# Kernel tuning notes

Measured on AMD Instinct MI355X. Metric: run time of the kernel, lower is better.

The kernel has to match this reference:

```python
import jax, jax.numpy as jnp
import numpy as np

HEADS = 16
DIM_HEAD = 64


def setup_inputs() -> dict:
    key = jax.random.key(0)
    k1, k2, k3 = jax.random.split(key, 3)
    b, n, dim = 4, 2048, 1024
    inner = HEADS * DIM_HEAD  # 1024
    x = jax.random.normal(k1, (b, n, dim), dtype=jnp.float32)
    # Dense weights, scaled like Glorot-ish init to keep softmax well-behaved
    w_qkv = jax.random.normal(k2, (dim, 3 * inner), dtype=jnp.float32) * (dim ** -0.5)
    w_out = jax.random.normal(k3, (inner, dim), dtype=jnp.float32) * (inner ** -0.5)
    b_out = jnp.zeros((dim,), dtype=jnp.float32)
    return {"x": x, "w_qkv": w_qkv, "w_out": w_out, "b_out": b_out}


def reference(x, w_qkv, w_out, b_out):
    b, n, dim = x.shape
    scale = DIM_HEAD ** -0.5
    qkv = x @ w_qkv  # [b, n, 3*h*d]
    q, k, v = jnp.split(qkv, 3, axis=-1)
    # 'b n (h d) -> b h n d'
    split_heads = lambda t: t.reshape(b, n, HEADS, DIM_HEAD).transpose(0, 2, 1, 3)
    q, k, v = split_heads(q), split_heads(k), split_heads(v)
    sim = jnp.einsum('bhid,bhjd->bhij', q, k) * scale  # [b, h, n, n]
    attn = jax.nn.softmax(sim, axis=-1)
    out = jnp.einsum('bhij,bhjd->bhid', attn, v)  # [b, h, n, d]
    out = out.transpose(0, 2, 1, 3).reshape(b, n, HEADS * DIM_HEAD)
    return out @ w_out + b_out  # dropout rate 0.0 -> identity
```

## Files before the change

kernel.cpp:

```cpp
#include <hip/hip_runtime.h>
#include <cstdint>

#define HEADS 16
#define DH 64
#define SEQ 2048
#define BATCH 4
#define DIM 1024
#define MTOT (BATCH*SEQ)
#define NQKV (3*DIM)

typedef short bf16x8 __attribute__((ext_vector_type(8)));
typedef float f32x4 __attribute__((ext_vector_type(4)));
typedef float f32x16 __attribute__((ext_vector_type(16)));

__device__ __forceinline__ unsigned short f2bf(float f) {
  union { float fv; unsigned int u; } c; c.fv = f;
  unsigned int u = c.u;
  u += 0x7FFFu + ((u >> 16) & 1u);
  return (unsigned short)(u >> 16);
}

__device__ __forceinline__ unsigned int cvtpk(float lo, float hi) {
  unsigned int r;
  asm("v_cvt_pk_bf16_f32 %0, %1, %2" : "=v"(r) : "v"(lo), "v"(hi));
  return r;
}

__device__ __forceinline__ f32x4 mfma16(bf16x8 a, bf16x8 b, f32x4 c) {
  return __builtin_amdgcn_mfma_f32_16x16x32_bf16(a, b, c, 0, 0, 0);
}
__device__ __forceinline__ f32x16 mfma32(bf16x8 a, bf16x8 b, f32x16 c) {
  return __builtin_amdgcn_mfma_f32_32x32x16_bf16(a, b, c, 0, 0, 0);
}

typedef const __attribute__((address_space(1))) unsigned int* gas_ptr;
typedef __attribute__((address_space(3))) unsigned int* las_ptr;
__device__ __forceinline__ void gl2lds16(const void* g, void* l) {
  __builtin_amdgcn_global_load_lds((gas_ptr)g, (las_ptr)l, 16, 0, 0);
}

#define QSCALE 0.18033688011112042f

__global__ __launch_bounds__(256) void cast_f32_bf16(
    const float* __restrict__ in, unsigned short* __restrict__ out, int n4) {
  int i = blockIdx.x * blockDim.x + threadIdx.x;
  if (i >= n4) return;
  float4 v = reinterpret_cast<const float4*>(in)[i];
  uint2 o;
  o.x = (unsigned int)f2bf(v.x) | ((unsigned int)f2bf(v.y) << 16);
  o.y = (unsigned int)f2bf(v.z) | ((unsigned int)f2bf(v.w) << 16);
  reinterpret_cast<uint2*>(out)[i] = o;
}

__global__ __launch_bounds__(256) void transpose_cast(
    const float* __restrict__ in, unsigned short* __restrict__ out, int R, int C) {
  __shared__ float tile[32][33];
  int c0 = blockIdx.x * 32, r0 = blockIdx.y * 32;
  int tx = threadIdx.x & 31, ty = threadIdx.x >> 5;
  for (int i = 0; i < 32; i += 8)
    tile[ty + i][tx] = in[(size_t)(r0 + ty + i) * C + c0 + tx];
  __syncthreads();
  for (int i = 0; i < 32; i += 8)
    out[(size_t)(c0 + ty + i) * R + r0 + tx] = f2bf(tile[tx][ty + i]);
}

__global__ __launch_bounds__(256) void transpose_v(
    const unsigned short* __restrict__ V, unsigned short* __restrict__ Vt) {
  __shared__ unsigned short tile[64][72];
  int n0 = blockIdx.x * 64;
  size_t base = (size_t)blockIdx.y * SEQ * DH;
  int t = threadIdx.x;
  int r = t >> 2, c = (t & 3) * 8;
  *(uint4*)&tile[r][c]      = *(const uint4*)&V[base + (size_t)(n0 + r) * DH + c];
  *(uint4*)&tile[r][c + 32] = *(const uint4*)&V[base + (size_t)(n0 + r) * DH + c + 32];
  __syncthreads();
#pragma unroll
  for (int p = 0; p < 2; p++) {
    alignas(16) unsigned short tmp[8];
#pragma unroll
    for (int i = 0; i < 8; i++) tmp[i] = tile[c + p * 32 + i][r];
    *(uint4*)&Vt[base + (size_t)r * SEQ + n0 + c + p * 32] = *(uint4*)tmp;
  }
}


#define STAGE(TT) { \
    char* _b = (char*)smem + ((TT) & 3) * 24576 + w * 1024; \
    gl2lds16(gA0 + (size_t)(TT) * 32, _b); \
    gl2lds16(gA1 + (size_t)(TT) * 32, _b + 8192); \
    gl2lds16(gB0 + (size_t)(TT) * 32, _b + 16384); }

#define WAITB(N) { \
    asm volatile("s_waitcnt vmcnt(" #N ")" ::: "memory"); \
    __builtin_amdgcn_s_barrier(); \
    __builtin_amdgcn_sched_barrier(0); }

#define GCOMPUTE(T) { \
    const unsigned short* sAt = smem + ((T) & 3) * 12288; \
    const unsigned short* sBt = sAt + 8192; \
    bf16x8 af[4], bv[4]; \
    _Pragma("unroll") \
    for (int mt = 0; mt < 4; mt++) \
      af[mt] = *reinterpret_cast<const bf16x8*>( \
          &sAt[(wr64 + mt * 16 + fr) * 32 + fchunk]); \
    _Pragma("unroll") \
    for (int nt = 0; nt < 4; nt++) \
      bv[nt] = *reinterpret_cast<const bf16x8*>( \
          &sBt[(wc64 + nt * 16 + fr) * 32 + fchunk]); \
    __builtin_amdgcn_s_setprio(1); \
    _Pragma("unroll") \
    for (int mt = 0; mt < 4; mt++) \
      _Pragma("unroll") \
      for (int nt = 0; nt < 4; nt++) \
        acc[mt][nt] = mfma16(af[mt], bv[nt], acc[mt][nt]); \
    __builtin_amdgcn_s_setprio(0); }

#define GEMM_SETUP(Abase, Bbase) \
  const int KD = 1024; \
  int t = threadIdx.x; \
  int lane = t & 63, w = t >> 6; \
  int wr64 = (w >> 1) * 64;            \
  int wc64 = (w & 1) * 64;             \
  int fr = lane & 15, fg = lane >> 4; \
  int fchunk = (fg ^ ((fr >> 1) & 3)) * 8;    \
  int lr = lane >> 2; \
  int cg = ((lane & 3) ^ ((lane >> 3) & 3)) * 8;   \
  const unsigned short* gA0 = (Abase) + (size_t)(m0 + w * 16 + lr) * KD + cg; \
  const unsigned short* gA1 = gA0 + (size_t)128 * KD; \
  const unsigned short* gB0 = (Bbase) + (size_t)(n0 + w * 16 + lr) * KD + cg; \
  f32x4 acc[4][4]; \
  _Pragma("unroll") \
  for (int i = 0; i < 4; i++) \
    _Pragma("unroll") \
    for (int j = 0; j < 4; j++) { f32x4 z = {0.f, 0.f, 0.f, 0.f}; acc[i][j] = z; }

#define GEMM_MAINLOOP \
  STAGE(0); STAGE(1); STAGE(2); \
  for (int kt = 0; kt < 30; ++kt) { \
    WAITB(6); \
    if (kt < 29) STAGE(kt + 3); \
    GCOMPUTE(kt); \
  } \
  WAITB(3); \
  GCOMPUTE(30); \
  WAITB(0); \
  GCOMPUTE(31);

__global__ __launch_bounds__(512, 2) void gemm_qkv(
    const unsigned short* __restrict__ A, const unsigned short* __restrict__ Bt,
    unsigned short* __restrict__ Q, unsigned short* __restrict__ K,
    unsigned short* __restrict__ V) {
  __shared__ unsigned short smem[4 * 12288];
  int gid = blockIdx.x + 24 * blockIdx.y;
  int swz = (gid & 7) * 96 + (gid >> 3);
  int m0 = (swz / 24) * 256;
  int n0 = (swz % 24) * 128;

  GEMM_SETUP(A, Bt)
  GEMM_MAINLOOP

  int rowq = fg * 4;
  int b = m0 >> 11;
  int nrow0 = (m0 & 2047) + wr64 + rowq;
#pragma unroll
  for (int nt = 0; nt < 4; nt++) {
    int ncb = n0 + wc64 + nt * 16;
    int which = ncb >> 10;
    int hdb = ncb & 1023;
    int hh = hdb >> 6;
    int dcol = (hdb & 63) + fr;
    unsigned short* dst = (which == 0) ? Q : (which == 1 ? K : V);
    size_t cbase = ((size_t)(b * HEADS + hh) * SEQ) * DH + dcol;
#pragma unroll
    for (int mt = 0; mt < 4; mt++) {
      f32x4 av = acc[mt][nt];
      if (which == 0) {
        av[0] *= QSCALE; av[1] *= QSCALE; av[2] *= QSCALE; av[3] *= QSCALE;
      }
      size_t idx = cbase + (size_t)(nrow0 + mt * 16) * DH;
      unsigned int u0 = cvtpk(av[0], av[1]);
      unsigned int u1 = cvtpk(av[2], av[3]);
      dst[idx]          = (unsigned short)u0;
      dst[idx + DH]     = (unsigned short)(u0 >> 16);
      dst[idx + 2 * DH] = (unsigned short)u1;
      dst[idx + 3 * DH] = (unsigned short)(u1 >> 16);
    }
  }
}

__global__ __launch_bounds__(512, 2) void gemm_out(
    const unsigned short* __restrict__ A, const unsigned short* __restrict__ Bt,
    const float* __restrict__ bias, float* __restrict__ C) {
  __shared__ unsigned short smem[4 * 12288];
  int gid = blockIdx.x + 8 * blockIdx.y;
  int swz = (gid & 7) * 32 + (gid >> 3);
  int m0 = (swz / 8) * 256;
  int n0 = (swz % 8) * 128;

  GEMM_SETUP(A, Bt)
  GEMM_MAINLOOP

  int rowq = fg * 4;
#pragma unroll
  for (int nt = 0; nt < 4; nt++) {
    int ncol = n0 + wc64 + nt * 16 + fr;
    float bb = bias[ncol];
    size_t cb = (size_t)(m0 + wr64 + rowq) * DIM + ncol;
#pragma unroll
    for (int mt = 0; mt < 4; mt++)
#pragma unroll
      for (int r = 0; r < 4; r++)
        C[cb + (size_t)(mt * 16 + r) * DIM] = acc[mt][nt][r] + bb;
  }
}

#define LDA 68

__global__ __launch_bounds__(256, 4) void attention(
    const unsigned short* __restrict__ Qg, const unsigned short* __restrict__ Kg,
    const unsigned short* __restrict__ Vtg, unsigned short* __restrict__ Og) {
  __shared__ unsigned short smem[2 * 64 * 72];
  unsigned short* sK  = smem;
  unsigned short* sVt = smem + 64 * LDA;

  int gid = blockIdx.x + 16 * (blockIdx.y + 16 * blockIdx.z);
  int qb   = (gid >> 3) & 15;
  int pair = ((gid & 7) << 3) | (gid >> 7);
  int h = pair & 15, b = pair >> 4;

  size_t base = (size_t)(b * HEADS + h) * SEQ * DH;
  const unsigned short* Q = Qg + base;
  const unsigned short* K = Kg + base;
  const unsigned short* Vt = Vtg + base;
  int t = threadIdx.x, lane = t & 63, w = t >> 6;
  int m = lane & 31, kh = lane >> 5;
  int q0 = qb * 128 + w * 32;

  bf16x8 qf[4];
#pragma unroll
  for (int kt = 0; kt < 4; kt++)
    qf[kt] = *reinterpret_cast<const bf16x8*>(
        &Q[(size_t)(q0 + m) * DH + kt * 16 + kh * 8]);

  f32x16 oaccT[2];
#pragma unroll
  for (int dh = 0; dh < 2; dh++)
#pragma unroll
    for (int i = 0; i < 16; i++) oaccT[dh][i] = 0.f;
  float rs = 0.f;

  int sr = t >> 2, sc = (t & 3) * 8;

  for (int j0 = 0; j0 < SEQ; j0 += 64) {
    {
      uint4 a0 = *(const uint4*)&K[(size_t)(j0 + sr) * DH + sc];
      uint4 a1 = *(const uint4*)&K[(size_t)(j0 + sr) * DH + sc + 32];
      uint4 b0 = *(const uint4*)&Vt[(size_t)sr * SEQ + j0 + sc];
      uint4 b1 = *(const uint4*)&Vt[(size_t)sr * SEQ + j0 + sc + 32];
      unsigned short* pk0 = &sK[sr * LDA + sc];
      unsigned short* pk1 = &sK[sr * LDA + sc + 32];
      unsigned short* pv0 = &sVt[sr * LDA + sc];
      unsigned short* pv1 = &sVt[sr * LDA + sc + 32];
      *(uint2*)pk0       = make_uint2(a0.x, a0.y);
      *(uint2*)(pk0 + 4) = make_uint2(a0.z, a0.w);
      *(uint2*)pk1       = make_uint2(a1.x, a1.y);
      *(uint2*)(pk1 + 4) = make_uint2(a1.z, a1.w);
      *(uint2*)pv0       = make_uint2(b0.x, b0.y);
      *(uint2*)(pv0 + 4) = make_uint2(b0.z, b0.w);
      *(uint2*)pv1       = make_uint2(b1.x, b1.y);
      *(uint2*)(pv1 + 4) = make_uint2(b1.z, b1.w);
    }
    __syncthreads();

    unsigned int pp[8][2];
#pragma unroll
    for (int jt = 0; jt < 2; jt++) {
      bf16x8 kf[4];
#pragma unroll
      for (int kt = 0; kt < 4; kt++) {
        union { uint2 u[2]; bf16x8 v; } kc;
        const unsigned short* p = &sK[(jt * 32 + m) * LDA + (2 * kt + kh) * 8];
        kc.u[0] = *(const uint2*)p;
        kc.u[1] = *(const uint2*)(p + 4);
        kf[kt] = kc.v;
      }
      f32x16 s;
#pragma unroll
      for (int i = 0; i < 16; i++) s[i] = 0.f;
#pragma unroll
      for (int kt = 0; kt < 4; kt++)
        s = mfma32(kf[kt], qf[kt], s);
      float e[16];
#pragma unroll
      for (int i = 0; i < 16; i++) e[i] = __builtin_amdgcn_exp2f(s[i]);
      float t0 = (e[0] + e[1]) + (e[2] + e[3]);
      float t1 = (e[4] + e[5]) + (e[6] + e[7]);
      float t2 = (e[8] + e[9]) + (e[10] + e[11]);
      float t3 = (e[12] + e[13]) + (e[14] + e[15]);
      rs += (t0 + t1) + (t2 + t3);
#pragma unroll
      for (int sl = 0; sl < 4; sl++) {
        pp[4 * jt + sl][0] = cvtpk(e[4 * sl + 0], e[4 * sl + 1]);
        pp[4 * jt + sl][1] = cvtpk(e[4 * sl + 2], e[4 * sl + 3]);
      }
    }

#pragma unroll
    for (int kb = 0; kb < 4; kb++) {
#pragma unroll
      for (int dh = 0; dh < 2; dh++) {
        union { uint2 u[2]; bf16x8 v; } ac;
        const unsigned short* p = &sVt[(32 * dh + m) * LDA + 16 * kb + 4 * kh];
        ac.u[0] = *(const uint2*)p;
        ac.u[1] = *(const uint2*)(p + 8);
        union { unsigned int u[4]; bf16x8 v; } bc;
        bc.u[0] = pp[2 * kb][0];
        bc.u[1] = pp[2 * kb][1];
        bc.u[2] = pp[2 * kb + 1][0];
        bc.u[3] = pp[2 * kb + 1][1];
        oaccT[dh] = mfma32(ac.v, bc.v, oaccT[dh]);
      }
    }
    __syncthreads();
  }

  float inv;
  {
    float tot = rs + __shfl_xor(rs, 32);
    inv = 1.0f / tot;
  }

  unsigned int* ew = (unsigned int*)smem + (size_t)w * 32 * 36;
#pragma unroll
  for (int dh = 0; dh < 2; dh++)
#pragma unroll
    for (int sl = 0; sl < 4; sl++) {
      unsigned int u0 = cvtpk(oaccT[dh][4 * sl + 0] * inv, oaccT[dh][4 * sl + 1] * inv);
      unsigned int u1 = cvtpk(oaccT[dh][4 * sl + 2] * inv, oaccT[dh][4 * sl + 3] * inv);
      uint2 pk; pk.x = u0; pk.y = u1;
      *(uint2*)&ew[m * 36 + 16 * dh + 4 * sl + 2 * kh] = pk;
    }
  {
    int mr = lane >> 3, ch = lane & 7;
#pragma unroll
    for (int it = 0; it < 4; it++) {
      uint4 vv = *(const uint4*)&ew[(8 * it + mr) * 36 + ch * 4];
      int n = q0 + 8 * it + mr;
      *(uint4*)&Og[((size_t)(b * SEQ + n)) * DIM + h * DH + ch * 8] = vv;
    }
  }
}

extern "C" void kernel_launch(void* const* d_in, const int* in_sizes, int n_in,
                              void* d_out, int out_size, void* d_ws, size_t ws_size,
                              hipStream_t stream) {
  const float* x     = (const float*)d_in[0];
  const float* w_qkv = (const float*)d_in[1];
  const float* w_out = (const float*)d_in[2];
  const float* b_out = (const float*)d_in[3];
  float* out = (float*)d_out;

  char* ws = (char*)d_ws;
  unsigned short* xb     = (unsigned short*)ws; ws += (size_t)MTOT * DIM * 2;
  unsigned short* wqkv_t = (unsigned short*)ws; ws += (size_t)NQKV * DIM * 2;
  unsigned short* wout_t = (unsigned short*)ws; ws += (size_t)DIM * DIM * 2;
  unsigned short* qb_    = (unsigned short*)ws; ws += (size_t)BATCH * HEADS * SEQ * DH * 2;
  unsigned short* kb_    = (unsigned short*)ws; ws += (size_t)BATCH * HEADS * SEQ * DH * 2;
  unsigned short* vb_    = (unsigned short*)ws; ws += (size_t)BATCH * HEADS * SEQ * DH * 2;
  unsigned short* attnb  = (unsigned short*)ws; ws += (size_t)MTOT * DIM * 2;
  unsigned short* vt_    = xb;

  cast_f32_bf16<<<(MTOT * DIM / 4 + 255) / 256, 256, 0, stream>>>(x, xb, MTOT * DIM / 4);
  transpose_cast<<<dim3(NQKV / 32, DIM / 32), 256, 0, stream>>>(w_qkv, wqkv_t, DIM, NQKV);
  transpose_cast<<<dim3(DIM / 32, DIM / 32), 256, 0, stream>>>(w_out, wout_t, DIM, DIM);

  gemm_qkv<<<dim3(24, 32), 512, 0, stream>>>(xb, wqkv_t, qb_, kb_, vb_);

  transpose_v<<<dim3(SEQ / 64, BATCH * HEADS), 256, 0, stream>>>(vb_, vt_);

  attention<<<dim3(SEQ / 128, HEADS, BATCH), 256, 0, stream>>>(qb_, kb_, vt_, attnb);

  gemm_out<<<dim3(8, 32), 512, 0, stream>>>(attnb, wout_t, b_out, out);
}
```

Before: 270.7 us.

## Restructure GEMM pipeline with K=64 tiles, fuse V transpose, prioritize attention MFMAs

```diff
diff --git a/kernel.cpp b/kernel.cpp
--- a/kernel.cpp
+++ b/kernel.cpp
@@ -64,49 +64,45 @@
     out[(size_t)(c0 + ty + i) * R + r0 + tx] = f2bf(tile[tx][ty + i]);
 }
 
-__global__ __launch_bounds__(256) void transpose_v(
-    const unsigned short* __restrict__ V, unsigned short* __restrict__ Vt) {
-  __shared__ unsigned short tile[64][72];
-  int n0 = blockIdx.x * 64;
-  size_t base = (size_t)blockIdx.y * SEQ * DH;
-  int t = threadIdx.x;
-  int r = t >> 2, c = (t & 3) * 8;
-  *(uint4*)&tile[r][c]      = *(const uint4*)&V[base + (size_t)(n0 + r) * DH + c];
-  *(uint4*)&tile[r][c + 32] = *(const uint4*)&V[base + (size_t)(n0 + r) * DH + c + 32];
-  __syncthreads();
-#pragma unroll
-  for (int p = 0; p < 2; p++) {
-    alignas(16) unsigned short tmp[8];
-#pragma unroll
-    for (int i = 0; i < 8; i++) tmp[i] = tile[c + p * 32 + i][r];
-    *(uint4*)&Vt[base + (size_t)r * SEQ + n0 + c + p * 32] = *(uint4*)tmp;
-  }
-}
-
-
-#define STAGE(TT) { \
-    char* _b = (char*)smem + ((TT) & 3) * 24576 + w * 1024; \
-    gl2lds16(gA0 + (size_t)(TT) * 32, _b); \
-    gl2lds16(gA1 + (size_t)(TT) * 32, _b + 8192); \
-    gl2lds16(gB0 + (size_t)(TT) * 32, _b + 16384); }
-
-#define WAITB(N) { \
-    asm volatile("s_waitcnt vmcnt(" #N ")" ::: "memory"); \
-    __builtin_amdgcn_s_barrier(); \
-    __builtin_amdgcn_sched_barrier(0); }
-
-#define GCOMPUTE(T) { \
-    const unsigned short* sAt = smem + ((T) & 3) * 12288; \
-    const unsigned short* sBt = sAt + 8192; \
+
+#define PG_SETUP(Abase, Bbase) \
+  int t = threadIdx.x; \
+  int lane = t & 63, w = t >> 6; \
+  int wm64 = (w >> 1) * 64, wn64 = (w & 1) * 64; \
+  int fr = lane & 15, fg = lane >> 4; \
+  const unsigned short* gAs = (Abase) + (size_t)(m0 + (t >> 3)) * 1024 \
+                              + ((t & 7) ^ ((t >> 3) & 7)) * 8; \
+  const unsigned short* gBs = (Bbase) + (size_t)(n0 + (t >> 3)) * 1024 \
+                              + ((t & 7) ^ ((t >> 3) & 7)) * 8; \
+  char* lds_c = (char*)smem + t * 16; \
+  f32x4 acc[4][4]; \
+  _Pragma("unroll") \
+  for (int i = 0; i < 4; i++) \
+    _Pragma("unroll") \
+    for (int j = 0; j < 4; j++) { f32x4 z = {0.f, 0.f, 0.f, 0.f}; acc[i][j] = z; }
+
+#define PG_STAGE_AH(SB, TT, H) { \
+    gl2lds16(gAs + (H) * 128 * 1024 + (TT) * 64, \
+             lds_c + (SB) * 49152 + (H) * 16384); \
+    gl2lds16(gAs + ((H) * 128 + 64) * 1024 + (TT) * 64, \
+             lds_c + (SB) * 49152 + (H) * 16384 + 8192); }
+
+#define PG_STAGE_B(SB, TT) { \
+    gl2lds16(gBs + (TT) * 64, lds_c + (SB) * 49152 + 32768); \
+    gl2lds16(gBs + 64 * 1024 + (TT) * 64, lds_c + (SB) * 49152 + 32768 + 8192); }
+
+#define PG_PHASE(SB, KS) { \
+    const unsigned short* sAb = smem + (SB) * 24576; \
+    const unsigned short* sBb = sAb + 16384; \
     bf16x8 af[4], bv[4]; \
     _Pragma("unroll") \
     for (int mt = 0; mt < 4; mt++) \
       af[mt] = *reinterpret_cast<const bf16x8*>( \
-          &sAt[(wr64 + mt * 16 + fr) * 32 + fchunk]); \
+          &sAb[(wm64 + mt * 16 + fr) * 64 + (((KS) * 4 + fg) ^ (fr & 7)) * 8]); \
     _Pragma("unroll") \
     for (int nt = 0; nt < 4; nt++) \
       bv[nt] = *reinterpret_cast<const bf16x8*>( \
-          &sBt[(wc64 + nt * 16 + fr) * 32 + fchunk]); \
+          &sBb[(wn64 + nt * 16 + fr) * 64 + (((KS) * 4 + fg) ^ (fr & 7)) * 8]); \
     __builtin_amdgcn_s_setprio(1); \
     _Pragma("unroll") \
     for (int mt = 0; mt < 4; mt++) \
@@ -115,97 +111,109 @@
         acc[mt][nt] = mfma16(af[mt], bv[nt], acc[mt][nt]); \
     __builtin_amdgcn_s_setprio(0); }
 
-#define GEMM_SETUP(Abase, Bbase) \
-  const int KD = 1024; \
-  int t = threadIdx.x; \
-  int lane = t & 63, w = t >> 6; \
-  int wr64 = (w >> 1) * 64;            \
-  int wc64 = (w & 1) * 64;             \
-  int fr = lane & 15, fg = lane >> 4; \
-  int fchunk = (fg ^ ((fr >> 1) & 3)) * 8;    \
-  int lr = lane >> 2; \
-  int cg = ((lane & 3) ^ ((lane >> 3) & 3)) * 8;   \
-  const unsigned short* gA0 = (Abase) + (size_t)(m0 + w * 16 + lr) * KD + cg; \
-  const unsigned short* gA1 = gA0 + (size_t)128 * KD; \
-  const unsigned short* gB0 = (Bbase) + (size_t)(n0 + w * 16 + lr) * KD + cg; \
-  f32x4 acc[4][4]; \
-  _Pragma("unroll") \
-  for (int i = 0; i < 4; i++) \
-    _Pragma("unroll") \
-    for (int j = 0; j < 4; j++) { f32x4 z = {0.f, 0.f, 0.f, 0.f}; acc[i][j] = z; }
-
-#define GEMM_MAINLOOP \
-  STAGE(0); STAGE(1); STAGE(2); \
-  for (int kt = 0; kt < 30; ++kt) { \
-    WAITB(6); \
-    if (kt < 29) STAGE(kt + 3); \
-    GCOMPUTE(kt); \
-  } \
-  WAITB(3); \
-  GCOMPUTE(30); \
-  WAITB(0); \
-  GCOMPUTE(31);
-
-__global__ __launch_bounds__(512, 2) void gemm_qkv(
+#define PG_MAIN { \
+    PG_STAGE_AH(0, 0, 0); PG_STAGE_AH(0, 0, 1); PG_STAGE_B(0, 0); \
+    PG_STAGE_AH(1, 1, 0); PG_STAGE_AH(1, 1, 1); PG_STAGE_B(1, 1); \
+    int buf = 0, sb = 2; \
+    _Pragma("unroll 1") \
+    for (int T = 0; T < 15; ++T) { \
+      asm volatile("s_waitcnt vmcnt(6)" ::: "memory"); \
+      __builtin_amdgcn_s_barrier(); \
+      __builtin_amdgcn_sched_barrier(0); \
+      if (T < 14) PG_STAGE_AH(sb, T + 2, 0); \
+      PG_PHASE(buf, 0); \
+      __builtin_amdgcn_s_barrier(); \
+      if (T < 14) { PG_STAGE_AH(sb, T + 2, 1); PG_STAGE_B(sb, T + 2); } \
+      PG_PHASE(buf, 1); \
+      buf = (buf == 2) ? 0 : buf + 1; \
+      sb = (sb == 2) ? 0 : sb + 1; \
+    } \
+    asm volatile("s_waitcnt vmcnt(0)" ::: "memory"); \
+    __builtin_amdgcn_s_barrier(); \
+    __builtin_amdgcn_sched_barrier(0); \
+    PG_PHASE(0, 0);  \
+    PG_PHASE(0, 1); }
+
+__global__ __launch_bounds__(512) void gemm_qkv(
     const unsigned short* __restrict__ A, const unsigned short* __restrict__ Bt,
     unsigned short* __restrict__ Q, unsigned short* __restrict__ K,
     unsigned short* __restrict__ V) {
-  __shared__ unsigned short smem[4 * 12288];
+  __shared__ unsigned short smem[73728];
   int gid = blockIdx.x + 24 * blockIdx.y;
   int swz = (gid & 7) * 96 + (gid >> 3);
   int m0 = (swz / 24) * 256;
   int n0 = (swz % 24) * 128;
 
-  GEMM_SETUP(A, Bt)
-  GEMM_MAINLOOP
+  PG_SETUP(A, Bt)
+  PG_MAIN
 
   int rowq = fg * 4;
   int b = m0 >> 11;
-  int nrow0 = (m0 & 2047) + wr64 + rowq;
+  int nrow0 = (m0 & 2047) + wm64 + rowq;
 #pragma unroll
   for (int nt = 0; nt < 4; nt++) {
-    int ncb = n0 + wc64 + nt * 16;
+    int ncb = n0 + wn64 + nt * 16;
     int which = ncb >> 10;
     int hdb = ncb & 1023;
     int hh = hdb >> 6;
-    int dcol = (hdb & 63) + fr;
-    unsigned short* dst = (which == 0) ? Q : (which == 1 ? K : V);
-    size_t cbase = ((size_t)(b * HEADS + hh) * SEQ) * DH + dcol;
-#pragma unroll
-    for (int mt = 0; mt < 4; mt++) {
-      f32x4 av = acc[mt][nt];
-      if (which == 0) {
-        av[0] *= QSCALE; av[1] *= QSCALE; av[2] *= QSCALE; av[3] *= QSCALE;
-      }
-      size_t idx = cbase + (size_t)(nrow0 + mt * 16) * DH;
-      unsigned int u0 = cvtpk(av[0], av[1]);
-      unsigned int u1 = cvtpk(av[2], av[3]);
-      dst[idx]          = (unsigned short)u0;
-      dst[idx + DH]     = (unsigned short)(u0 >> 16);
-      dst[idx + 2 * DH] = (unsigned short)u1;
-      dst[idx + 3 * DH] = (unsigned short)(u1 >> 16);
-    }
-  }
-}
-
-__global__ __launch_bounds__(512, 2) void gemm_out(
+    if (which == 2) {
+      unsigned short* tw = smem + 24576 + ((nt & 1) ? 9216 : 0) + w * 1152;
+#pragma unroll
+      for (int mt = 0; mt < 4; mt++) {
+        f32x4 av = acc[mt][nt];
+        uint2 pk;
+        pk.x = cvtpk(av[0], av[1]);
+        pk.y = cvtpk(av[2], av[3]);
+        *(uint2*)&tw[fr * 72 + mt * 16 + fg * 4] = pk;
+      }
+      int dr = lane >> 2, sg = lane & 3;
+      size_t vrow = ((size_t)(b * HEADS + hh) * DH + nt * 16 + dr) * SEQ
+                  + (m0 & 2047) + wm64 + sg * 8;
+#pragma unroll
+      for (int it = 0; it < 2; it++) {
+        uint4 vv = *(const uint4*)&tw[dr * 72 + sg * 8 + it * 32];
+        *(uint4*)&V[vrow + it * 32] = vv;
+      }
+    } else {
+      int dcol = (hdb & 63) + fr;
+      unsigned short* dst = (which == 0) ? Q : K;
+      size_t cbase = ((size_t)(b * HEADS + hh) * SEQ) * DH + dcol;
+#pragma unroll
+      for (int mt = 0; mt < 4; mt++) {
+        f32x4 av = acc[mt][nt];
+        if (which == 0) {
+          av[0] *= QSCALE; av[1] *= QSCALE; av[2] *= QSCALE; av[3] *= QSCALE;
+        }
+        size_t idx = cbase + (size_t)(nrow0 + mt * 16) * DH;
+        unsigned int u0 = cvtpk(av[0], av[1]);
+        unsigned int u1 = cvtpk(av[2], av[3]);
+        dst[idx]          = (unsigned short)u0;
+        dst[idx + DH]     = (unsigned short)(u0 >> 16);
+        dst[idx + 2 * DH] = (unsigned short)u1;
+        dst[idx + 3 * DH] = (unsigned short)(u1 >> 16);
+      }
+    }
+  }
+}
+
+__global__ __launch_bounds__(512) void gemm_out(
     const unsigned short* __restrict__ A, const unsigned short* __restrict__ Bt,
     const float* __restrict__ bias, float* __restrict__ C) {
-  __shared__ unsigned short smem[4 * 12288];
+  __shared__ unsigned short smem[73728];
   int gid = blockIdx.x + 8 * blockIdx.y;
   int swz = (gid & 7) * 32 + (gid >> 3);
   int m0 = (swz / 8) * 256;
   int n0 = (swz % 8) * 128;
 
-  GEMM_SETUP(A, Bt)
-  GEMM_MAINLOOP
+  PG_SETUP(A, Bt)
+  PG_MAIN
 
   int rowq = fg * 4;
 #pragma unroll
   for (int nt = 0; nt < 4; nt++) {
-    int ncol = n0 + wc64 + nt * 16 + fr;
+    int ncol = n0 + wn64 + nt * 16 + fr;
     float bb = bias[ncol];
-    size_t cb = (size_t)(m0 + wr64 + rowq) * DIM + ncol;
+    size_t cb = (size_t)(m0 + wm64 + rowq) * DIM + ncol;
 #pragma unroll
     for (int mt = 0; mt < 4; mt++)
 #pragma unroll
@@ -287,9 +295,11 @@
       f32x16 s;
 #pragma unroll
       for (int i = 0; i < 16; i++) s[i] = 0.f;
+      __builtin_amdgcn_s_setprio(1);
 #pragma unroll
       for (int kt = 0; kt < 4; kt++)
         s = mfma32(kf[kt], qf[kt], s);
+      __builtin_amdgcn_s_setprio(0);
       float e[16];
 #pragma unroll
       for (int i = 0; i < 16; i++) e[i] = __builtin_amdgcn_exp2f(s[i]);
@@ -305,6 +315,7 @@
       }
     }
 
+    __builtin_amdgcn_s_setprio(1);
 #pragma unroll
     for (int kb = 0; kb < 4; kb++) {
 #pragma unroll
@@ -321,6 +332,7 @@
         oaccT[dh] = mfma32(ac.v, bc.v, oaccT[dh]);
       }
     }
+    __builtin_amdgcn_s_setprio(0);
     __syncthreads();
   }
 
@@ -366,19 +378,16 @@
   unsigned short* wout_t = (unsigned short*)ws; ws += (size_t)DIM * DIM * 2;
   unsigned short* qb_    = (unsigned short*)ws; ws += (size_t)BATCH * HEADS * SEQ * DH * 2;
   unsigned short* kb_    = (unsigned short*)ws; ws += (size_t)BATCH * HEADS * SEQ * DH * 2;
-  unsigned short* vb_    = (unsigned short*)ws; ws += (size_t)BATCH * HEADS * SEQ * DH * 2;
+  unsigned short* vtb_   = (unsigned short*)ws; ws += (size_t)BATCH * HEADS * SEQ * DH * 2;
   unsigned short* attnb  = (unsigned short*)ws; ws += (size_t)MTOT * DIM * 2;
-  unsigned short* vt_    = xb;
 
   cast_f32_bf16<<<(MTOT * DIM / 4 + 255) / 256, 256, 0, stream>>>(x, xb, MTOT * DIM / 4);
   transpose_cast<<<dim3(NQKV / 32, DIM / 32), 256, 0, stream>>>(w_qkv, wqkv_t, DIM, NQKV);
   transpose_cast<<<dim3(DIM / 32, DIM / 32), 256, 0, stream>>>(w_out, wout_t, DIM, DIM);
 
-  gemm_qkv<<<dim3(24, 32), 512, 0, stream>>>(xb, wqkv_t, qb_, kb_, vb_);
-
-  transpose_v<<<dim3(SEQ / 64, BATCH * HEADS), 256, 0, stream>>>(vb_, vt_);
-
-  attention<<<dim3(SEQ / 128, HEADS, BATCH), 256, 0, stream>>>(qb_, kb_, vt_, attnb);
+  gemm_qkv<<<dim3(24, 32), 512, 0, stream>>>(xb, wqkv_t, qb_, kb_, vtb_);
+
+  attention<<<dim3(SEQ / 128, HEADS, BATCH), 256, 0, stream>>>(qb_, kb_, vtb_, attnb);
 
   gemm_out<<<dim3(8, 32), 512, 0, stream>>>(attnb, wout_t, b_out, out);
 }
```

Result: no change. 266.3 us (-1.6%).
